# Performance work log

Hardware: AMD Instinct MI355X
Metric: run time of the kernel (lower is better)

The kernel has to match this reference:

```python
import jax, jax.numpy as jnp
import numpy as np
import math

B, C, H, W = 8, 64, 128, 128
OUT, HEADS, K, S = 32, 8, 3, 2
DH = C // HEADS
PAD = (K - 1) // 2
EPS = 1e-5


def _unfold(t, k):
    # t: [B, C, H, W] -> per-pixel kxk windows [B*H*W, k*k, C] (torch.nn.Unfold layout: channel-major)
    b, c, h, w = t.shape
    pat = jax.lax.conv_general_dilated_patches(t, (k, k), (1, 1), [(PAD, PAD), (PAD, PAD)])  # [B, C*k*k, H, W]
    pat = pat.reshape(b, c, k * k, h * w)          # [B, C, k^2, HW]
    return jnp.transpose(pat, (0, 3, 2, 1)).reshape(b * h * w, k * k, c)


def setup_inputs() -> dict:
    key = jax.random.key(0)
    ks = jax.random.split(key, 18)
    def n(k, shape, sc=0.05):
        return jax.random.normal(k, shape, jnp.float32) * sc
    return {
        "x": jax.random.normal(ks[0], (B, C, H, W), jnp.float32),
        "up_query": jax.random.normal(ks[1], (1, S * S, C), jnp.float32),  # learned up-sampling queries
        "Wk": n(ks[2], (C, C)), "bk": n(ks[3], (C,), 0.02),   # to_k 1x1 conv
        "Wv": n(ks[4], (C, C)), "bv": n(ks[5], (C,), 0.02),   # to_v 1x1 conv
        "Wq": n(ks[6], (C, C)), "bq": n(ks[7], (C,), 0.02),   # MHA q proj
        "Wka": n(ks[8], (C, C)), "bka": n(ks[9], (C,), 0.02), # MHA k proj
        "Wva": n(ks[10], (C, C)), "bva": n(ks[11], (C,), 0.02),  # MHA v proj
        "Wo": n(ks[12], (C, OUT)), "bo": n(ks[13], (OUT,), 0.02),  # MHA output proj (project_dim=out_dim)
        "rel_pos": n(ks[14], (1, HEADS, S * S, K * K), 1.0),  # learned relative positional bias
        "ln_g": jnp.ones((OUT,), jnp.float32),
        "ln_b": jnp.zeros((OUT,), jnp.float32),
    }


def reference(x, up_query, Wk, bk, Wv, bv, Wq, bq, Wka, bka, Wva, bva, Wo, bo, rel_pos, ln_g, ln_b):
    b, c, h, w = x.shape
    # pre_norm = Identity (post_norm=True). pe_k = Identity (pos_embedding=None).
    kf = jnp.einsum('bchw,cd->bdhw', x, Wk) + bk[None, :, None, None]
    vf = jnp.einsum('bchw,cd->bdhw', x, Wv) + bv[None, :, None, None]
    # aux_zeros branch: to_k(pe(zeros)) == conv bias -> adds bk to every window position
    xk = _unfold(kf, K) + bk[None, None, :]            # [N, k^2, C]
    xv = _unfold(vf, K)                                # [N, k^2, C]
    n = xk.shape[0]
    xq = jnp.broadcast_to(up_query, (n, S * S, c))     # [N, s^2, C]
    # multi-head attention with relative positional bias on logits
    qh = (xq @ Wq + bq).reshape(n, S * S, HEADS, DH)
    kh = (xk @ Wka + bka).reshape(n, K * K, HEADS, DH)
    vh = (xv @ Wva + bva).reshape(n, K * K, HEADS, DH)
    logits = jnp.einsum('nqhd,nkhd->nhqk', qh, kh) / math.sqrt(DH) + rel_pos  # [N, h, s^2, k^2]
    attn = jax.nn.softmax(logits, axis=-1)
    out = jnp.einsum('nhqk,nkhd->nqhd', attn, vh).reshape(n, S * S, c)
    out = out @ Wo + bo                                # [N, s^2, OUT]
    # post LayerNorm over out_dim
    mu = jnp.mean(out, axis=-1, keepdims=True)
    var = jnp.mean(jnp.square(out - mu), axis=-1, keepdims=True)
    out = (out - mu) / jnp.sqrt(var + EPS) * ln_g + ln_b
    # pixel-shuffle style reshape to [B, OUT, H*s, W*s]
    out = out.reshape(b, h, w, S, S, OUT)
    out = jnp.transpose(out, (0, 5, 1, 3, 2, 4)).reshape(b, OUT, h * S, w * S)
    return out
```

## Files before the change

kernel.cpp:

```cpp
#include <hip/hip_runtime.h>

#define HW    16384
#define WIDTH 128
#define LOG2E    1.4426950408889634f
#define RS_LOG2E 0.5101464200926166f

#define WFB_DWORDS 4992
#define WOT_OFF    4992
#define REL_OFF    6016
#define WS_DWORDS  6304

typedef short bshort8 __attribute__((ext_vector_type(8)));
typedef _Float16 half8 __attribute__((ext_vector_type(8)));
typedef float f32x4   __attribute__((ext_vector_type(4)));
typedef unsigned u32x4 __attribute__((ext_vector_type(4)));
typedef unsigned u32x2 __attribute__((ext_vector_type(2)));

static __device__ inline unsigned short f2bf(float f) {
    unsigned u = __builtin_bit_cast(unsigned, f);
    unsigned r = u + 0x7fff + ((u >> 16) & 1);
    return (unsigned short)(r >> 16);
}
static __device__ inline unsigned cvtpk(float lo, float hi) {
    unsigned d;
    asm("v_cvt_pk_bf16_f32 %0, %1, %2" : "=v"(d) : "v"(lo), "v"(hi));
    return d;
}
static __device__ inline unsigned pkrtz(float lo, float hi) {
    return __builtin_bit_cast(unsigned, __builtin_amdgcn_cvt_pkrtz(lo, hi));
}
static __device__ inline float lo16f(unsigned u) {
    return (float)__builtin_bit_cast(_Float16, (unsigned short)(u & 0xffffu));
}
static __device__ inline float hi16f(unsigned u) {
    return (float)__builtin_bit_cast(_Float16, (unsigned short)(u >> 16));
}
static __device__ inline unsigned pkfma16_lo(unsigned o, unsigned a, unsigned v) {
    asm("v_pk_fma_f16 %0, %1, %2, %0 op_sel:[0,0,0] op_sel_hi:[0,1,1]"
        : "+v"(o) : "v"(a), "v"(v));
    return o;
}
static __device__ inline unsigned pkfma16_hi(unsigned o, unsigned a, unsigned v) {
    asm("v_pk_fma_f16 %0, %1, %2, %0 op_sel:[1,0,0] op_sel_hi:[1,1,1]"
        : "+v"(o) : "v"(a), "v"(v));
    return o;
}
static __device__ inline unsigned pkmul16_lo(unsigned a, unsigned r) {
    unsigned d;
    asm("v_pk_mul_f16 %0, %1, %2 op_sel:[0,0] op_sel_hi:[0,1]"
        : "=v"(d) : "v"(r), "v"(a));
    return d;
}
static __device__ inline unsigned pkmul16_hi(unsigned a, unsigned r) {
    unsigned d;
    asm("v_pk_mul_f16 %0, %1, %2 op_sel:[1,0] op_sel_hi:[1,1]"
        : "=v"(d) : "v"(r), "v"(a));
    return d;
}

__global__ __launch_bounds__(256) void k0_fuse(
    const float* __restrict__ up_query,
    const float* __restrict__ Wk, const float* __restrict__ bk,
    const float* __restrict__ Wv, const float* __restrict__ bv,
    const float* __restrict__ Wq, const float* __restrict__ bq,
    const float* __restrict__ Wka, const float* __restrict__ bka,
    const float* __restrict__ Wva, const float* __restrict__ bva,
    const float* __restrict__ Wo, const float* __restrict__ rel_pos,
    float* __restrict__ ws)
{
    __shared__ float qcS[4][64];
    __shared__ float WkT[64][65];
    __shared__ float WvT[64][65];
    __shared__ float colS[12][64];
    __shared__ float bred[12][8];
    __shared__ float pred[12][8];

    const int tid = threadIdx.x;
    const int bj  = blockIdx.x;
    const int j0  = bj * 12;

    {
        int q = tid >> 6, f = tid & 63;
        float a = bq[f];
        for (int c = 0; c < 64; ++c) a = fmaf(up_query[q*64+c], Wq[c*64+f], a);
        qcS[q][f] = a;
    }
    for (int i = tid; i < 4096; i += 256) {
        int c = i >> 6, e = i & 63;
        WkT[e][c] = Wk[i];
        WvT[e][c] = Wv[i];
    }
    __syncthreads();

    for (int i = tid; i < 768; i += 256) {
        int jl = i >> 6, e = i & 63;
        int j = j0 + jl;
        float v;
        if (j < 32) {
            int h = j >> 2, qq = j & 3;
            float s = 0.f;
            #pragma unroll
            for (int d = 0; d < 8; ++d)
                s = fmaf(Wka[e*64 + h*8 + d], qcS[qq][h*8 + d], s);
            v = s * RS_LOG2E;
        } else {
            v = Wva[e*64 + (j - 32)];
        }
        colS[jl][e] = v;
    }
    if (tid < 96) {
        int jl = tid >> 3, d = tid & 7;
        int j = j0 + jl;
        if (j < 32) {
            int h = j >> 2, qq = j & 3;
            int fi = h*8 + d;
            float bW = 0.f;
            for (int e = 0; e < 64; ++e) bW = fmaf(bk[e], Wka[e*64 + fi], bW);
            float qv = qcS[qq][fi];
            bred[jl][d] = (2.f*bW + bka[fi]) * qv;
            pred[jl][d] = bW * qv;
        } else {
            float s = 0.f;
            for (int e = d*8; e < d*8 + 8; ++e)
                s = fmaf(bv[e], Wva[e*64 + (j - 32)], s);
            bred[jl][d] = s;
            pred[jl][d] = 0.f;
        }
    }
    __syncthreads();

    unsigned* wsd = (unsigned*)ws;
    for (int i = tid; i < 384; i += 256) {
        int cp = i & 31, jl = i >> 5;
        int j = j0 + jl;
        const float (*MT)[65] = (j < 32) ? WkT : WvT;
        float o0 = 0.f, o1 = 0.f;
        for (int e = 0; e < 64; ++e) {
            float cv = colS[jl][e];
            o0 = fmaf(MT[e][2*cp],     cv, o0);
            o1 = fmaf(MT[e][2*cp + 1], cv, o1);
        }
        wsd[j*52 + cp] = (unsigned)f2bf(o0) | ((unsigned)f2bf(o1) << 16);
    }
    for (int i = tid; i < 240; i += 256) {
        int jl = i / 20, kd = 32 + (i % 20);
        int j = j0 + jl;
        unsigned val = 0u;
        if (kd == 32) {
            float sv = 0.f, sp = 0.f;
            #pragma unroll
            for (int d = 0; d < 8; ++d) { sv += bred[jl][d]; sp += pred[jl][d]; }
            float bf_, pd_;
            if (j < 32) { bf_ = sv * RS_LOG2E; pd_ = (sv - sp) * RS_LOG2E; }
            else        { bf_ = sv + bva[j-32]; pd_ = bva[j-32]; }
            val = (unsigned)f2bf(bf_) | ((unsigned)f2bf(pd_) << 16);
        }
        wsd[j*52 + kd] = val;
    }
    if (bj == 7) {
        for (int i = tid; i < 1024; i += 256) {
            int col = i >> 5, kp = i & 31;
            wsd[WOT_OFF + i] = pkrtz(Wo[(2*kp)*32 + col], Wo[(2*kp + 1)*32 + col]);
        }
        for (int i = tid; i < 288; i += 256)
            ws[REL_OFF + i] = rel_pos[i] * LOG2E;
    }
}

__global__ __launch_bounds__(256, 5) void k2_attn(
    const float* __restrict__ x, const float* __restrict__ ws,
    const float* __restrict__ bo,
    const float* __restrict__ ln_g, const float* __restrict__ ln_b,
    float* __restrict__ out)
{
    __shared__ __align__(16) char smem[32768];

    const int tid = threadIdx.x;

    const int flat = blockIdx.x;
    const int wg   = (flat & 7) * 256 + (flat >> 3);
    const int tx = wg & 15;
    const int ty = (wg >> 4) & 15;
    const int b  = wg >> 8;

    #pragma unroll
    for (int it = 0; it < 3; ++it) {
        int i = tid + it*256;
        if (i < 600) {
            int kq = i / 50;
            int pp = i - kq*50;
            int p0 = pp*2;
            int py = p0/10; int px0 = p0 - py*10;
            int gy = ty*8 - 1 + py, gx0 = tx*8 - 1 + px0;
            bool vy = (unsigned)gy < 128u;
            bool v0 = vy && ((unsigned)gx0 < 128u);
            bool v1 = vy && ((unsigned)(gx0+1) < 128u);
            u32x4 pk0 = {0u,0u,0u,0u}, pk1 = {0u,0u,0u,0u};
            if (kq < 8) {
                const float* xp = x + ((size_t)b*64 + kq*8)*HW + gy*WIDTH + gx0;
                if (v0 && v1) {
                    #pragma unroll
                    for (int e = 0; e < 4; ++e) {
                        float2 c0 = *(const float2*)(xp + (size_t)(2*e)*HW);
                        float2 c1 = *(const float2*)(xp + (size_t)(2*e+1)*HW);
                        pk0[e] = cvtpk(c0.x, c1.x);
                        pk1[e] = cvtpk(c0.y, c1.y);
                    }
                } else if (v0 || v1) {
                    #pragma unroll
                    for (int e = 0; e < 4; ++e) {
                        float a0 = 0.f, b0 = 0.f, a1 = 0.f, b1 = 0.f;
                        if (v0) { a0 = xp[(size_t)(2*e)*HW];     b0 = xp[(size_t)(2*e+1)*HW]; }
                        if (v1) { a1 = xp[(size_t)(2*e)*HW + 1]; b1 = xp[(size_t)(2*e+1)*HW + 1]; }
                        pk0[e] = cvtpk(a0, b0);
                        pk1[e] = cvtpk(a1, b1);
                    }
                }
            } else if (kq == 8) {
                pk0[0] = v0 ? 0x00003f80u : 0x3f800000u;
                pk1[0] = v1 ? 0x00003f80u : 0x3f800000u;
            }
            char* dst = smem + kq*1792 + p0*16;
            *(u32x4*)(dst)      = pk0;
            *(u32x4*)(dst + 16) = pk1;
        }
    }
    __syncthreads();

    const int lane = tid & 63;
    const int wv   = tid >> 6;
    const int frow = lane & 15;
    const int kseg = lane >> 4;

    const unsigned short* wfs = (const unsigned short*)ws;
    f32x4 accs[12];
    __builtin_amdgcn_s_setprio(1);
    #pragma unroll
    for (int mi = 0; mi < 2; ++mi) {
        const int mt = wv*2 + mi;
        if (mt < 7) {
            const int prow = mt*16 + frow;
            bshort8 xa0 = *(const bshort8*)(smem + (0*4 + kseg)*1792 + prow*16);
            bshort8 xa1 = *(const bshort8*)(smem + (1*4 + kseg)*1792 + prow*16);
            bshort8 xa2 = *(const bshort8*)(smem + (2*4 + kseg)*1792 + prow*16);
            #pragma unroll
            for (int nt = 0; nt < 6; ++nt) {
                const unsigned short* wrow = wfs + (nt*16 + frow)*104 + kseg*8;
                f32x4 acc = {0.f, 0.f, 0.f, 0.f};
                acc = __builtin_amdgcn_mfma_f32_16x16x32_bf16(*(const bshort8*)(wrow),      xa0, acc, 0, 0, 0);
                acc = __builtin_amdgcn_mfma_f32_16x16x32_bf16(*(const bshort8*)(wrow + 32), xa1, acc, 0, 0, 0);
                acc = __builtin_amdgcn_mfma_f32_16x16x32_bf16(*(const bshort8*)(wrow + 64), xa2, acc, 0, 0, 0);
                accs[mi*6 + nt] = acc;
            }
        }
    }
    __builtin_amdgcn_s_setprio(0);
    __syncthreads();

    unsigned short* Lh = (unsigned short*)smem;
    char*           Vb = smem + 8192;
    #pragma unroll
    for (int mi = 0; mi < 2; ++mi) {
        const int mt = wv*2 + mi;
        if (mt < 7) {
            const int p = mt*16 + frow;
            if (p < 100) {
                #pragma unroll
                for (int nt = 0; nt < 6; ++nt) {
                    const f32x4 acc = accs[mi*6 + nt];
                    u32x2 dd = { pkrtz(acc[0], acc[1]), pkrtz(acc[2], acc[3]) };
                    if (nt < 2) {
                        *(u32x2*)(Lh + p*36 + nt*16 + kseg*4) = dd;
                    } else {
                        *(u32x2*)(Vb + p*144 + (nt-2)*32 + kseg*8) = dd;
                    }
                }
            }
        }
    }
    __syncthreads();

    const int dpy = lane >> 3, dpx = lane & 7;
    const int pbase = dpy*10 + dpx;
    const float* relw = ws + REL_OFF;

    unsigned od[32];
    #pragma unroll
    for (int hh = 0; hh < 2; ++hh) {
        const int h = wv*2 + hh;
        unsigned apk[2][9];
        float s0 = 0.f, s1 = 0.f, s2 = 0.f, s3 = 0.f;
        const float* rp = relw + h*36;
        const unsigned short* lbase = Lh + pbase*36 + h*4;
        #pragma unroll
        for (int n = 0; n < 9; ++n) {
            const int off = (n/3)*10 + (n%3);
            const u32x2 L4 = *(const u32x2*)(lbase + off*36);
            float e0 = exp2f(lo16f(L4[0]) + rp[n]);
            float e1 = exp2f(hi16f(L4[0]) + rp[9 + n]);
            float e2 = exp2f(lo16f(L4[1]) + rp[18 + n]);
            float e3 = exp2f(hi16f(L4[1]) + rp[27 + n]);
            s0 += e0; s1 += e1; s2 += e2; s3 += e3;
            apk[0][n] = pkrtz(e0, e1);
            apk[1][n] = pkrtz(e2, e3);
        }
        const unsigned r01 = pkrtz(__builtin_amdgcn_rcpf(s0), __builtin_amdgcn_rcpf(s1));
        const unsigned r23 = pkrtz(__builtin_amdgcn_rcpf(s2), __builtin_amdgcn_rcpf(s3));

        unsigned o16[4][4] = {{0u,0u,0u,0u},{0u,0u,0u,0u},{0u,0u,0u,0u},{0u,0u,0u,0u}};
        const char* vbase = Vb + pbase*144 + h*16;
        __builtin_amdgcn_s_setprio(1);
        #pragma unroll
        for (int n = 0; n < 9; ++n) {
            const int off = (n/3)*10 + (n%3);
            const u32x4 v4 = *(const u32x4*)(vbase + off*144);
            #pragma unroll
            for (int j = 0; j < 4; ++j) {
                o16[0][j] = pkfma16_lo(o16[0][j], apk[0][n], v4[j]);
                o16[1][j] = pkfma16_hi(o16[1][j], apk[0][n], v4[j]);
                o16[2][j] = pkfma16_lo(o16[2][j], apk[1][n], v4[j]);
                o16[3][j] = pkfma16_hi(o16[3][j], apk[1][n], v4[j]);
            }
        }
        __builtin_amdgcn_s_setprio(0);
        #pragma unroll
        for (int j = 0; j < 4; ++j) {
            od[(0*2 + hh)*4 + j] = pkmul16_lo(o16[0][j], r01);
            od[(1*2 + hh)*4 + j] = pkmul16_hi(o16[1][j], r01);
            od[(2*2 + hh)*4 + j] = pkmul16_lo(o16[2][j], r23);
            od[(3*2 + hh)*4 + j] = pkmul16_hi(o16[3][j], r23);
        }
    }
    __syncthreads();

    {
        const unsigned sw = ((unsigned)(lane & 7)) << 4;
        #pragma unroll
        for (int q = 0; q < 4; ++q) {
            const int row = lane*4 + q;
            #pragma unroll
            for (int hh = 0; hh < 2; ++hh) {
                u32x4 w4 = { od[(q*2+hh)*4+0], od[(q*2+hh)*4+1],
                             od[(q*2+hh)*4+2], od[(q*2+hh)*4+3] };
                *(u32x4*)(smem + row*128 + (((unsigned)(wv*32 + hh*16)) ^ sw)) = w4;
            }
        }
    }
    __syncthreads();

    const unsigned short* wotu = (const unsigned short*)ws + WOT_OFF*2;
    half8 av[4][2];
    #pragma unroll
    for (int mt = 0; mt < 4; ++mt) {
        const int row = wv*64 + mt*16 + frow;
        const unsigned sw = (((unsigned)(row >> 2)) & 7u) << 4;
        #pragma unroll
        for (int ks = 0; ks < 2; ++ks)
            av[mt][ks] = __builtin_bit_cast(half8,
                *(const u32x4*)(smem + row*128 + (((unsigned)(kseg*16 + ks*64)) ^ sw)));
    }
    half8 bv_[2][2];
    #pragma unroll
    for (int nt = 0; nt < 2; ++nt) {
        const int col = nt*16 + frow;
        #pragma unroll
        for (int ks = 0; ks < 2; ++ks)
            bv_[nt][ks] = __builtin_bit_cast(half8,
                *(const u32x4*)(wotu + col*64 + kseg*8 + ks*32));
    }
    f32x4 cacc[4][2];
    #pragma unroll
    for (int mt = 0; mt < 4; ++mt)
        #pragma unroll
        for (int nt = 0; nt < 2; ++nt)
            cacc[mt][nt] = (f32x4){0.f, 0.f, 0.f, 0.f};
    __builtin_amdgcn_s_setprio(1);
    #pragma unroll
    for (int ks = 0; ks < 2; ++ks)
        #pragma unroll
        for (int mt = 0; mt < 4; ++mt)
            #pragma unroll
            for (int nt = 0; nt < 2; ++nt)
                cacc[mt][nt] = __builtin_amdgcn_mfma_f32_16x16x32_f16(
                    av[mt][ks], bv_[nt][ks], cacc[mt][nt], 0, 0, 0);
    __builtin_amdgcn_s_setprio(0);

    #pragma unroll
    for (int mt = 0; mt < 4; ++mt)
        #pragma unroll
        for (int nt = 0; nt < 2; ++nt)
            #pragma unroll
            for (int r = 0; r < 4; ++r) {
                const int row = wv*64 + mt*16 + kseg*4 + r;
                const int col = nt*16 + frow;
                *(float*)(smem + row*128
                    + (((unsigned)(col*4)) ^ ((((unsigned)(row >> 2)) & 7u) << 4)))
                    = cacc[mt][nt][r];
            }
    asm volatile("s_waitcnt lgkmcnt(0)" ::: "memory");

    float cv[32];
    {
        const unsigned sw = (((unsigned)(tid >> 2)) & 7u) << 4;
        #pragma unroll
        for (int j = 0; j < 8; ++j) {
            const f32x4 c4 = *(const f32x4*)(smem + tid*128 + (((unsigned)(j*16)) ^ sw));
            cv[j*4+0] = c4[0]; cv[j*4+1] = c4[1]; cv[j*4+2] = c4[2]; cv[j*4+3] = c4[3];
        }
    }
    float mu = 0.f;
    #pragma unroll
    for (int oc = 0; oc < 32; ++oc) { cv[oc] += bo[oc]; mu += cv[oc]; }
    mu *= (1.f/32.f);
    float var = 0.f;
    #pragma unroll
    for (int oc = 0; oc < 32; ++oc) { float d = cv[oc] - mu; var += d*d; }
    var *= (1.f/32.f);
    const float rstd = rsqrtf(var + 1e-5f);

    const int q   = tid & 3;
    const int pix = tid >> 2;
    const int gy = ty*8 + (pix >> 3), gx = tx*8 + (pix & 7);
    const int Y = gy*2 + (q >> 1), X = gx*2 + (q & 1);
    float* op = out + (((size_t)b*32)*256 + Y)*256 + X;
    #pragma unroll
    for (int oc = 0; oc < 32; ++oc) {
        float v = (cv[oc] - mu) * rstd * ln_g[oc] + ln_b[oc];
        op[(size_t)oc * 65536] = v;
    }
}

extern "C" void kernel_launch(void* const* d_in, const int* in_sizes, int n_in,
                              void* d_out, int out_size, void* d_ws, size_t ws_size,
                              hipStream_t stream)
{
    const float* x        = (const float*)d_in[0];
    const float* up_query = (const float*)d_in[1];
    const float* Wk  = (const float*)d_in[2];
    const float* bk  = (const float*)d_in[3];
    const float* Wv  = (const float*)d_in[4];
    const float* bv  = (const float*)d_in[5];
    const float* Wq  = (const float*)d_in[6];
    const float* bq  = (const float*)d_in[7];
    const float* Wka = (const float*)d_in[8];
    const float* bka = (const float*)d_in[9];
    const float* Wva = (const float*)d_in[10];
    const float* bva = (const float*)d_in[11];
    const float* Wo  = (const float*)d_in[12];
    const float* bo  = (const float*)d_in[13];
    const float* rel_pos = (const float*)d_in[14];
    const float* ln_g = (const float*)d_in[15];
    const float* ln_b = (const float*)d_in[16];

    float* ws  = (float*)d_ws;
    float* out = (float*)d_out;

    if (ws_size < (size_t)WS_DWORDS * 4) return;

    k0_fuse<<<8, 256, 0, stream>>>(up_query, Wk, bk, Wv, bv, Wq, bq,
                                   Wka, bka, Wva, bva, Wo, rel_pos, ws);
    k2_attn<<<2048, 256, 0, stream>>>(x, ws, bo, ln_g, ln_b, out);
}
```

Baseline: 65.05 us.

## Move bias out of MFMA K-dim, shrink LDS, split output stage into two passes

```diff
diff --git a/kernel.cpp b/kernel.cpp
--- a/kernel.cpp
+++ b/kernel.cpp
@@ -5,10 +5,12 @@
 #define LOG2E    1.4426950408889634f
 #define RS_LOG2E 0.5101464200926166f
 
-#define WFB_DWORDS 4992
-#define WOT_OFF    4992
-#define REL_OFF    6016
-#define WS_DWORDS  6304
+#define WFB_DWORDS 3072
+#define BIASV_OFF  3072
+#define BIASP_OFF  3168
+#define WOT_OFF    3264
+#define REL_OFF    4288
+#define WS_DWORDS  4576
 
 typedef short bshort8 __attribute__((ext_vector_type(8)));
 typedef _Float16 half8 __attribute__((ext_vector_type(8)));
@@ -140,22 +142,18 @@
             o0 = fmaf(MT[e][2*cp],     cv, o0);
             o1 = fmaf(MT[e][2*cp + 1], cv, o1);
         }
-        wsd[j*52 + cp] = (unsigned)f2bf(o0) | ((unsigned)f2bf(o1) << 16);
-    }
-    for (int i = tid; i < 240; i += 256) {
-        int jl = i / 20, kd = 32 + (i % 20);
-        int j = j0 + jl;
-        unsigned val = 0u;
-        if (kd == 32) {
-            float sv = 0.f, sp = 0.f;
-            #pragma unroll
-            for (int d = 0; d < 8; ++d) { sv += bred[jl][d]; sp += pred[jl][d]; }
-            float bf_, pd_;
-            if (j < 32) { bf_ = sv * RS_LOG2E; pd_ = (sv - sp) * RS_LOG2E; }
-            else        { bf_ = sv + bva[j-32]; pd_ = bva[j-32]; }
-            val = (unsigned)f2bf(bf_) | ((unsigned)f2bf(pd_) << 16);
-        }
-        wsd[j*52 + kd] = val;
+        wsd[j*32 + cp] = (unsigned)f2bf(o0) | ((unsigned)f2bf(o1) << 16);
+    }
+    if (tid < 12) {
+        int j = j0 + tid;
+        float sv = 0.f, sp = 0.f;
+        #pragma unroll
+        for (int d = 0; d < 8; ++d) { sv += bred[tid][d]; sp += pred[tid][d]; }
+        float bV, bP;
+        if (j < 32) { bV = sv * RS_LOG2E; bP = (sv - sp) * RS_LOG2E; }
+        else        { bV = sv + bva[j-32]; bP = bva[j-32]; }
+        ws[BIASV_OFF + j] = bV;
+        ws[BIASP_OFF + j] = bP;
     }
     if (bj == 7) {
         for (int i = tid; i < 1024; i += 256) {
@@ -167,13 +165,13 @@
     }
 }
 
-__global__ __launch_bounds__(256, 5) void k2_attn(
+__global__ __launch_bounds__(256, 7) void k2_attn(
     const float* __restrict__ x, const float* __restrict__ ws,
     const float* __restrict__ bo,
     const float* __restrict__ ln_g, const float* __restrict__ ln_b,
     float* __restrict__ out)
 {
-    __shared__ __align__(16) char smem[32768];
+    __shared__ __align__(16) char smem[20000];
 
     const int tid = threadIdx.x;
 
@@ -184,10 +182,10 @@
     const int b  = wg >> 8;
 
     #pragma unroll
-    for (int it = 0; it < 3; ++it) {
+    for (int it = 0; it < 2; ++it) {
         int i = tid + it*256;
-        if (i < 600) {
-            int kq = i / 50;
+        if (i < 400) {
+            int kq = (int)(((unsigned)i * 5243u) >> 18);
             int pp = i - kq*50;
             int p0 = pp*2;
             int py = p0/10; int px0 = p0 - py*10;
@@ -196,29 +194,24 @@
             bool v0 = vy && ((unsigned)gx0 < 128u);
             bool v1 = vy && ((unsigned)(gx0+1) < 128u);
             u32x4 pk0 = {0u,0u,0u,0u}, pk1 = {0u,0u,0u,0u};
-            if (kq < 8) {
-                const float* xp = x + ((size_t)b*64 + kq*8)*HW + gy*WIDTH + gx0;
-                if (v0 && v1) {
-                    #pragma unroll
-                    for (int e = 0; e < 4; ++e) {
-                        float2 c0 = *(const float2*)(xp + (size_t)(2*e)*HW);
-                        float2 c1 = *(const float2*)(xp + (size_t)(2*e+1)*HW);
-                        pk0[e] = cvtpk(c0.x, c1.x);
-                        pk1[e] = cvtpk(c0.y, c1.y);
-                    }
-                } else if (v0 || v1) {
-                    #pragma unroll
-                    for (int e = 0; e < 4; ++e) {
-                        float a0 = 0.f, b0 = 0.f, a1 = 0.f, b1 = 0.f;
-                        if (v0) { a0 = xp[(size_t)(2*e)*HW];     b0 = xp[(size_t)(2*e+1)*HW]; }
-                        if (v1) { a1 = xp[(size_t)(2*e)*HW + 1]; b1 = xp[(size_t)(2*e+1)*HW + 1]; }
-                        pk0[e] = cvtpk(a0, b0);
-                        pk1[e] = cvtpk(a1, b1);
-                    }
+            const float* xp = x + ((size_t)b*64 + kq*8)*HW + gy*WIDTH + gx0;
+            if (v0 && v1) {
+                #pragma unroll
+                for (int e = 0; e < 4; ++e) {
+                    float2 c0 = *(const float2*)(xp + (size_t)(2*e)*HW);
+                    float2 c1 = *(const float2*)(xp + (size_t)(2*e+1)*HW);
+                    pk0[e] = cvtpk(c0.x, c1.x);
+                    pk1[e] = cvtpk(c0.y, c1.y);
                 }
-            } else if (kq == 8) {
-                pk0[0] = v0 ? 0x00003f80u : 0x3f800000u;
-                pk1[0] = v1 ? 0x00003f80u : 0x3f800000u;
+            } else if (v0 || v1) {
+                #pragma unroll
+                for (int e = 0; e < 4; ++e) {
+                    float a0 = 0.f, b0 = 0.f, a1 = 0.f, b1 = 0.f;
+                    if (v0) { a0 = xp[(size_t)(2*e)*HW];     b0 = xp[(size_t)(2*e+1)*HW]; }
+                    if (v1) { a1 = xp[(size_t)(2*e)*HW + 1]; b1 = xp[(size_t)(2*e+1)*HW + 1]; }
+                    pk0[e] = cvtpk(a0, b0);
+                    pk1[e] = cvtpk(a1, b1);
+                }
             }
             char* dst = smem + kq*1792 + p0*16;
             *(u32x4*)(dst)      = pk0;
@@ -234,7 +227,6 @@
 
     const unsigned short* wfs = (const unsigned short*)ws;
     f32x4 accs[12];
-    __builtin_amdgcn_s_setprio(1);
     #pragma unroll
     for (int mi = 0; mi < 2; ++mi) {
         const int mt = wv*2 + mi;
@@ -242,37 +234,45 @@
             const int prow = mt*16 + frow;
             bshort8 xa0 = *(const bshort8*)(smem + (0*4 + kseg)*1792 + prow*16);
             bshort8 xa1 = *(const bshort8*)(smem + (1*4 + kseg)*1792 + prow*16);
-            bshort8 xa2 = *(const bshort8*)(smem + (2*4 + kseg)*1792 + prow*16);
             #pragma unroll
             for (int nt = 0; nt < 6; ++nt) {
-                const unsigned short* wrow = wfs + (nt*16 + frow)*104 + kseg*8;
+                const unsigned short* wrow = wfs + (nt*16 + frow)*64 + kseg*8;
                 f32x4 acc = {0.f, 0.f, 0.f, 0.f};
                 acc = __builtin_amdgcn_mfma_f32_16x16x32_bf16(*(const bshort8*)(wrow),      xa0, acc, 0, 0, 0);
                 acc = __builtin_amdgcn_mfma_f32_16x16x32_bf16(*(const bshort8*)(wrow + 32), xa1, acc, 0, 0, 0);
-                acc = __builtin_amdgcn_mfma_f32_16x16x32_bf16(*(const bshort8*)(wrow + 64), xa2, acc, 0, 0, 0);
                 accs[mi*6 + nt] = acc;
             }
         }
     }
-    __builtin_amdgcn_s_setprio(0);
     __syncthreads();
 
     unsigned short* Lh = (unsigned short*)smem;
-    char*           Vb = smem + 8192;
+    char*           Vb = smem + 7200;
+    const float* biasV = ws + BIASV_OFF;
+    const float* biasP = ws + BIASP_OFF;
     #pragma unroll
     for (int mi = 0; mi < 2; ++mi) {
         const int mt = wv*2 + mi;
         if (mt < 7) {
             const int p = mt*16 + frow;
             if (p < 100) {
+                int py = p/10, px = p - py*10;
+                int gy = ty*8 - 1 + py, gx = tx*8 - 1 + px;
+                bool vld = ((unsigned)gy < 128u) && ((unsigned)gx < 128u);
+                const float* bb = vld ? biasV : biasP;
+                const unsigned vsw = ((unsigned)(p & 7)) << 4;
                 #pragma unroll
                 for (int nt = 0; nt < 6; ++nt) {
-                    const f32x4 acc = accs[mi*6 + nt];
+                    f32x4 acc = accs[mi*6 + nt];
+                    const f32x4 b4 = *(const f32x4*)(bb + nt*16 + kseg*4);
+                    acc[0] += b4[0]; acc[1] += b4[1];
+                    acc[2] += b4[2]; acc[3] += b4[3];
                     u32x2 dd = { pkrtz(acc[0], acc[1]), pkrtz(acc[2], acc[3]) };
                     if (nt < 2) {
                         *(u32x2*)(Lh + p*36 + nt*16 + kseg*4) = dd;
                     } else {
-                        *(u32x2*)(Vb + p*144 + (nt-2)*32 + kseg*8) = dd;
+                        unsigned off = ((unsigned)((nt-2)*32 + kseg*8)) ^ vsw;
+                        *(u32x2*)(Vb + p*128 + off) = dd;
                     }
                 }
             }
@@ -308,12 +308,11 @@
         const unsigned r23 = pkrtz(__builtin_amdgcn_rcpf(s2), __builtin_amdgcn_rcpf(s3));
 
         unsigned o16[4][4] = {{0u,0u,0u,0u},{0u,0u,0u,0u},{0u,0u,0u,0u},{0u,0u,0u,0u}};
-        const char* vbase = Vb + pbase*144 + h*16;
-        __builtin_amdgcn_s_setprio(1);
         #pragma unroll
         for (int n = 0; n < 9; ++n) {
-            const int off = (n/3)*10 + (n%3);
-            const u32x4 v4 = *(const u32x4*)(vbase + off*144);
+            const int pp = pbase + (n/3)*10 + (n%3);
+            const u32x4 v4 = *(const u32x4*)(Vb + pp*128
+                                 + (((unsigned)(h*16)) ^ (((unsigned)(pp & 7)) << 4)));
             #pragma unroll
             for (int j = 0; j < 4; ++j) {
                 o16[0][j] = pkfma16_lo(o16[0][j], apk[0][n], v4[j]);
@@ -322,7 +321,6 @@
                 o16[3][j] = pkfma16_hi(o16[3][j], apk[1][n], v4[j]);
             }
         }
-        __builtin_amdgcn_s_setprio(0);
         #pragma unroll
         for (int j = 0; j < 4; ++j) {
             od[(0*2 + hh)*4 + j] = pkmul16_lo(o16[0][j], r01);
@@ -333,100 +331,96 @@
     }
     __syncthreads();
 
-    {
-        const unsigned sw = ((unsigned)(lane & 7)) << 4;
-        #pragma unroll
-        for (int q = 0; q < 4; ++q) {
-            const int row = lane*4 + q;
-            #pragma unroll
-            for (int hh = 0; hh < 2; ++hh) {
-                u32x4 w4 = { od[(q*2+hh)*4+0], od[(q*2+hh)*4+1],
-                             od[(q*2+hh)*4+2], od[(q*2+hh)*4+3] };
-                *(u32x4*)(smem + row*128 + (((unsigned)(wv*32 + hh*16)) ^ sw)) = w4;
-            }
-        }
-    }
-    __syncthreads();
-
     const unsigned short* wotu = (const unsigned short*)ws + WOT_OFF*2;
-    half8 av[4][2];
-    #pragma unroll
-    for (int mt = 0; mt < 4; ++mt) {
-        const int row = wv*64 + mt*16 + frow;
-        const unsigned sw = (((unsigned)(row >> 2)) & 7u) << 4;
+    half8 bvv[2][2];
+    #pragma unroll
+    for (int nt = 0; nt < 2; ++nt)
         #pragma unroll
         for (int ks = 0; ks < 2; ++ks)
-            av[mt][ks] = __builtin_bit_cast(half8,
-                *(const u32x4*)(smem + row*128 + (((unsigned)(kseg*16 + ks*64)) ^ sw)));
-    }
-    half8 bv_[2][2];
-    #pragma unroll
-    for (int nt = 0; nt < 2; ++nt) {
-        const int col = nt*16 + frow;
-        #pragma unroll
-        for (int ks = 0; ks < 2; ++ks)
-            bv_[nt][ks] = __builtin_bit_cast(half8,
-                *(const u32x4*)(wotu + col*64 + kseg*8 + ks*32));
-    }
-    f32x4 cacc[4][2];
-    #pragma unroll
-    for (int mt = 0; mt < 4; ++mt)
-        #pragma unroll
-        for (int nt = 0; nt < 2; ++nt)
-            cacc[mt][nt] = (f32x4){0.f, 0.f, 0.f, 0.f};
-    __builtin_amdgcn_s_setprio(1);
-    #pragma unroll
-    for (int ks = 0; ks < 2; ++ks)
-        #pragma unroll
-        for (int mt = 0; mt < 4; ++mt)
+            bvv[nt][ks] = __builtin_bit_cast(half8,
+                *(const u32x4*)(wotu + (nt*16 + frow)*64 + kseg*8 + ks*32));
+
+    const unsigned swO = ((unsigned)(lane & 7)) << 4;
+    #pragma unroll
+    for (int pass = 0; pass < 2; ++pass) {
+        if ((lane >> 5) == pass) {
+            const int l31 = lane & 31;
+            #pragma unroll
+            for (int q = 0; q < 4; ++q) {
+                const int row = l31*4 + q;
+                #pragma unroll
+                for (int hh = 0; hh < 2; ++hh) {
+                    u32x4 w4 = { od[(q*2+hh)*4+0], od[(q*2+hh)*4+1],
+                                 od[(q*2+hh)*4+2], od[(q*2+hh)*4+3] };
+                    *(u32x4*)(smem + row*128 + (((unsigned)(wv*32 + hh*16)) ^ swO)) = w4;
+                }
+            }
+        }
+        __syncthreads();
+
+        f32x4 cacc[2][2];
+        #pragma unroll
+        for (int mtl = 0; mtl < 2; ++mtl)
             #pragma unroll
             for (int nt = 0; nt < 2; ++nt)
-                cacc[mt][nt] = __builtin_amdgcn_mfma_f32_16x16x32_f16(
-                    av[mt][ks], bv_[nt][ks], cacc[mt][nt], 0, 0, 0);
-    __builtin_amdgcn_s_setprio(0);
-
-    #pragma unroll
-    for (int mt = 0; mt < 4; ++mt)
-        #pragma unroll
-        for (int nt = 0; nt < 2; ++nt)
-            #pragma unroll
-            for (int r = 0; r < 4; ++r) {
-                const int row = wv*64 + mt*16 + kseg*4 + r;
-                const int col = nt*16 + frow;
-                *(float*)(smem + row*128
-                    + (((unsigned)(col*4)) ^ ((((unsigned)(row >> 2)) & 7u) << 4)))
-                    = cacc[mt][nt][r];
-            }
-    asm volatile("s_waitcnt lgkmcnt(0)" ::: "memory");
-
-    float cv[32];
-    {
-        const unsigned sw = (((unsigned)(tid >> 2)) & 7u) << 4;
-        #pragma unroll
-        for (int j = 0; j < 8; ++j) {
-            const f32x4 c4 = *(const f32x4*)(smem + tid*128 + (((unsigned)(j*16)) ^ sw));
-            cv[j*4+0] = c4[0]; cv[j*4+1] = c4[1]; cv[j*4+2] = c4[2]; cv[j*4+3] = c4[3];
-        }
-    }
-    float mu = 0.f;
-    #pragma unroll
-    for (int oc = 0; oc < 32; ++oc) { cv[oc] += bo[oc]; mu += cv[oc]; }
-    mu *= (1.f/32.f);
-    float var = 0.f;
-    #pragma unroll
-    for (int oc = 0; oc < 32; ++oc) { float d = cv[oc] - mu; var += d*d; }
-    var *= (1.f/32.f);
-    const float rstd = rsqrtf(var + 1e-5f);
-
-    const int q   = tid & 3;
-    const int pix = tid >> 2;
-    const int gy = ty*8 + (pix >> 3), gx = tx*8 + (pix & 7);
-    const int Y = gy*2 + (q >> 1), X = gx*2 + (q & 1);
-    float* op = out + (((size_t)b*32)*256 + Y)*256 + X;
-    #pragma unroll
-    for (int oc = 0; oc < 32; ++oc) {
-        float v = (cv[oc] - mu) * rstd * ln_g[oc] + ln_b[oc];
-        op[(size_t)oc * 65536] = v;
+                cacc[mtl][nt] = (f32x4){0.f, 0.f, 0.f, 0.f};
+        #pragma unroll
+        for (int mtl = 0; mtl < 2; ++mtl) {
+            const int rowa = wv*32 + mtl*16 + frow;
+            const unsigned swa = (((unsigned)(rowa >> 2)) & 7u) << 4;
+            #pragma unroll
+            for (int ks = 0; ks < 2; ++ks) {
+                half8 av = __builtin_bit_cast(half8,
+                    *(const u32x4*)(smem + rowa*128 + (((unsigned)(kseg*16 + ks*64)) ^ swa)));
+                cacc[mtl][0] = __builtin_amdgcn_mfma_f32_16x16x32_f16(av, bvv[0][ks], cacc[mtl][0], 0, 0, 0);
+                cacc[mtl][1] = __builtin_amdgcn_mfma_f32_16x16x32_f16(av, bvv[1][ks], cacc[mtl][1], 0, 0, 0);
+            }
+        }
+        #pragma unroll
+        for (int mtl = 0; mtl < 2; ++mtl)
+            #pragma unroll
+            for (int nt = 0; nt < 2; ++nt)
+                #pragma unroll
+                for (int r = 0; r < 4; ++r) {
+                    const int row = wv*32 + mtl*16 + kseg*4 + r;
+                    const int col = nt*16 + frow;
+                    *(float*)(smem + row*128
+                        + (((unsigned)(col*4)) ^ ((((unsigned)(row >> 2)) & 7u) << 4)))
+                        = cacc[mtl][nt][r];
+                }
+        __syncthreads();
+
+        if ((tid >> 7) == pass) {
+            const int brow = tid & 127;
+            float cv[32];
+            const unsigned sw = (((unsigned)(brow >> 2)) & 7u) << 4;
+            #pragma unroll
+            for (int j = 0; j < 8; ++j) {
+                const f32x4 c4 = *(const f32x4*)(smem + brow*128 + (((unsigned)(j*16)) ^ sw));
+                cv[j*4+0] = c4[0]; cv[j*4+1] = c4[1]; cv[j*4+2] = c4[2]; cv[j*4+3] = c4[3];
+            }
+            float mu = 0.f;
+            #pragma unroll
+            for (int oc = 0; oc < 32; ++oc) { cv[oc] += bo[oc]; mu += cv[oc]; }
+            mu *= (1.f/32.f);
+            float var = 0.f;
+            #pragma unroll
+            for (int oc = 0; oc < 32; ++oc) { float d = cv[oc] - mu; var += d*d; }
+            var *= (1.f/32.f);
+            const float rstd = rsqrtf(var + 1e-5f);
+
+            const int q   = tid & 3;
+            const int pix = tid >> 2;
+            const int gy = ty*8 + (pix >> 3), gx = tx*8 + (pix & 7);
+            const int Y = gy*2 + (q >> 1), X = gx*2 + (q & 1);
+            float* op = out + (((size_t)b*32)*256 + Y)*256 + X;
+            #pragma unroll
+            for (int oc = 0; oc < 32; ++oc) {
+                float v = (cv[oc] - mu) * rstd * ln_g[oc] + ln_b[oc];
+                op[(size_t)oc * 65536] = v;
+            }
+        }
+        __syncthreads();
     }
 }
 
```

Result: slower. 104.3 us (+60.3%).
